# Optimization experiments

Hardware: AMD Instinct MI355X
Metric: run time of the kernel (lower is better)

Reference implementation:

```python
import jax, jax.numpy as jnp
import numpy as np

B, T, D = 4, 2048, 1024
HEADS = 8
D_K = D // HEADS


def setup_inputs() -> dict:
    key = jax.random.key(0)
    kq, kk, kv = jax.random.split(key, 3)
    return {
        "query": jax.random.normal(kq, (B, T, D), dtype=jnp.float32),
        "key": jax.random.normal(kk, (B, T, D), dtype=jnp.float32),
        "value": jax.random.normal(kv, (B, T, D), dtype=jnp.float32),
    }


def reference(query, key, value):
    b, t, d = query.shape
    # [B,T,D] -> [B,H,T,d_k]
    q = query.reshape(b, t, HEADS, D_K).transpose(0, 2, 1, 3)
    k = key.reshape(b, t, HEADS, D_K).transpose(0, 2, 1, 3)
    v = value.reshape(b, t, HEADS, D_K).transpose(0, 2, 1, 3)
    scale = 1.0 / jnp.sqrt(jnp.asarray(D_K, dtype=q.dtype))
    scores = jnp.einsum("bhqd,bhkd->bhqk", q, k) * scale  # [B,H,T,T]
    p_attn = jax.nn.softmax(scores, axis=-1)
    # sharpening: second softmax over 1000*p, clamp to [0,1]
    attn = jnp.clip(jax.nn.softmax(1000.0 * p_attn, axis=-1), 0.0, 1.0)
    x = jnp.einsum("bhqk,bhkd->bhqd", attn, v)  # [B,H,T,d_k]
    out = x.transpose(0, 2, 1, 3).reshape(b, t, HEADS * D_K)
    return out
```

## Files before the change

### kernel.cpp

```cpp
#include <hip/hip_runtime.h>


typedef __attribute__((ext_vector_type(4))) float f32x4;
typedef __attribute__((ext_vector_type(8))) _Float16 h16x8;
typedef __attribute__((ext_vector_type(4))) _Float16 h16x4;
typedef __attribute__((ext_vector_type(8))) short s16x8;
typedef __attribute__((ext_vector_type(4))) short s16x4;
typedef __attribute__((ext_vector_type(2))) unsigned int u32x2;
typedef __attribute__((ext_vector_type(4))) unsigned int u32x4;

#define NB 4
#define T_ 2048
#define D_ 1024
#define NH 8
#define DK 128
#define BQ 64
#define NWG (NB * NH * (T_ / BQ))
#define KB2 32
#define NKC2 (T_ / KB2)
#define SCALE 0.08838834764831845f
#define SC2   0.12751741689839996f
#define MOFF2 11.541560327111707f
#define L2E   1.4426950408889634f

__device__ __forceinline__ unsigned int pk2(float a, float b) {
  return __builtin_bit_cast(unsigned int, __builtin_amdgcn_cvt_pkrtz(a, b));
}
#define H8(p) __builtin_bit_cast(h16x8, *(const s16x8*)(p))

__device__ __forceinline__ void gload16(const unsigned short* g, unsigned short* l) {
  __builtin_amdgcn_global_load_lds(
      (const __attribute__((address_space(1))) void*)g,
      (__attribute__((address_space(3))) void*)l, 16, 0, 0);
}

__global__ __launch_bounds__(256) void cvtK16(const float* __restrict__ Kg,
                                              unsigned short* __restrict__ K16) {
  const int t = threadIdx.x;
#pragma unroll
  for (int i = 0; i < 4; ++i) {
    const unsigned gid = blockIdx.x * 1024u + i * 256u + t;
    const unsigned bhk = gid >> 4, dg = gid & 15u;
    const unsigned b = bhk >> 14, rem = bhk & 16383u;
    const unsigned h = rem >> 11, k = rem & 2047u;
    const float* s = Kg + ((size_t)b * T_ + k) * D_ + h * DK + dg * 8;
    f32x4 x0 = *(const f32x4*)s, x1 = *(const f32x4*)(s + 4);
    h16x8 hv;
#pragma unroll
    for (int j = 0; j < 4; ++j) { hv[j] = (_Float16)x0[j]; hv[j + 4] = (_Float16)x1[j]; }
    *(u32x4*)(K16 + (size_t)gid * 8) = __builtin_bit_cast(u32x4, hv);
  }
}

__global__ __launch_bounds__(256) void trV16(const float* __restrict__ Vg,
                                             unsigned short* __restrict__ V16t) {
  __shared__ float vt[64][129];
  const int t = threadIdx.x;
  const int bh = blockIdx.x >> 5;
  const int kc = blockIdx.x & 31;
  const int b = bh >> 3, h = bh & 7;
  const float* src = Vg + ((size_t)b * T_ + kc * 64) * D_ + h * DK;
#pragma unroll
  for (int p = 0; p < 8; ++p) {
    const int j = t + p * 256;
    const int row = j >> 5, c4 = j & 31;
    f32x4 v = *(const f32x4*)(src + (size_t)row * D_ + c4 * 4);
#pragma unroll
    for (int i = 0; i < 4; ++i) vt[row][c4 * 4 + i] = v[i];
  }
  __syncthreads();
  unsigned short* dst = V16t + (size_t)bh * DK * T_ + (size_t)kc * 64;
#pragma unroll
  for (int i = 0; i < 4; ++i) {
    const int gg = t + i * 256;
    const int d = gg >> 3, kg = gg & 7;
    u32x4 pv;
#pragma unroll
    for (int jj = 0; jj < 4; ++jj)
      pv[jj] = pk2(vt[kg * 8 + 2 * jj][d], vt[kg * 8 + 2 * jj + 1][d]);
    *(u32x4*)(dst + (size_t)d * T_ + kg * 8) = pv;
  }
}

__global__ __launch_bounds__(256, 4) void simattn_v7(
    const float* __restrict__ Qg, const unsigned short* __restrict__ K16,
    const unsigned short* __restrict__ V16t, float* __restrict__ Og) {
  __shared__ __align__(16) unsigned short kf[2][KB2 * DK];
  __shared__ __align__(16) unsigned short vts[2][DK * KB2];

  const int tid  = threadIdx.x;
  const int wid  = tid >> 6;
  const int lane = tid & 63;
  const int lr   = lane & 15;
  const int lg   = lane >> 4;

  const int blk  = (blockIdx.x & 7) * (NWG >> 3) + (blockIdx.x >> 3);
  const int qblk = blk & (T_ / BQ - 1);
  const int h    = (blk >> 5) & (NH - 1);
  const int b    = blk >> 8;
  const int q0   = qblk * BQ;
  const size_t bh  = (size_t)b * (T_ * D_) + (size_t)h * DK;
  const int    bhp = b * NH + h;
  const unsigned short* kp16 = K16 + (size_t)bhp * (T_ * DK);
  const unsigned short* vp16 = V16t + (size_t)bhp * (DK * T_);

  h16x8 qf[4];
  {
    const float* qp = Qg + bh + (size_t)(q0 + wid * 16 + lr) * D_;
#pragma unroll
    for (int s = 0; s < 4; ++s) {
      const int d0 = s * 32 + lg * 8;
      f32x4 x0 = *(const f32x4*)(qp + d0);
      f32x4 x1 = *(const f32x4*)(qp + d0 + 4);
#pragma unroll
      for (int i = 0; i < 4; ++i) {
        qf[s][i]     = (_Float16)x0[i];
        qf[s][i + 4] = (_Float16)x1[i];
      }
    }
  }

  int koffs[2], voffs[2];
  const int kdst0 = wid * 1024;
#pragma unroll
  for (int i = 0; i < 2; ++i) {
    const int id = wid * 2 + i;
    {
      const int r = id * 4 + (lane >> 4), gL = lane & 15;
      koffs[i] = r * DK + ((gL ^ (r & 7)) * 8);
    }
    {
      const int d = id * 16 + (lane >> 2), s = lane & 3;
      voffs[i] = d * T_ + ((s ^ ((d >> 1) & 3)) * 8);
    }
  }
  auto stK = [&](int kc, int buf) {
    const unsigned short* s0 = kp16 + (size_t)kc * (KB2 * DK);
    gload16(s0 + koffs[0], &kf[buf][kdst0]);
    gload16(s0 + koffs[1], &kf[buf][kdst0 + 512]);
  };
  auto stV = [&](int kc, int buf) {
    const unsigned short* s0 = vp16 + kc * KB2;
    gload16(s0 + voffs[0], &vts[buf][kdst0]);
    gload16(s0 + voffs[1], &vts[buf][kdst0 + 512]);
  };

  auto qkT = [&](int buf, f32x4* st) {
    st[0] = (f32x4){0.f, 0.f, 0.f, 0.f};
    st[1] = (f32x4){0.f, 0.f, 0.f, 0.f};
#pragma unroll
    for (int s = 0; s < 4; ++s) {
#pragma unroll
      for (int nt = 0; nt < 2; ++nt) {
        const int kr = nt * 16 + lr;
        const int eg = ((4 * s + lg) ^ (kr & 7)) * 8;
        st[nt] = __builtin_amdgcn_mfma_f32_16x16x32_f16(
            H8(&kf[buf][kr * DK + eg]), qf[s], st[nt], 0, 0, 0);
      }
    }
  };

  float msc = -3.0e38f, l8 = 0.f;
  stK(0, 0);
  __syncthreads();
  for (int kc = 0; kc < NKC2; ++kc) {
    if (kc + 1 < NKC2) stK(kc + 1, (kc + 1) & 1);
    f32x4 st[2];
    qkT(kc & 1, st);
    float e[8];
#pragma unroll
    for (int nt = 0; nt < 2; ++nt) {
#pragma unroll
      for (int r = 0; r < 4; ++r) {
        const float s = st[nt][r];
        msc = fmaxf(msc, s);
        e[nt * 4 + r] = __builtin_amdgcn_exp2f(fmaf(s, SC2, -MOFF2));
      }
    }
    l8 += ((e[0] + e[1]) + (e[2] + e[3])) + ((e[4] + e[5]) + (e[6] + e[7]));
    __syncthreads();
  }
  msc = fmaxf(msc, __shfl_xor(msc, 16));
  msc = fmaxf(msc, __shfl_xor(msc, 32));
  l8 += __shfl_xor(l8, 16);
  l8 += __shfl_xor(l8, 32);
  const float pm   = __builtin_amdgcn_exp2f(fmaf(msc, SC2, -MOFF2));
  const float ul2  = (1000.0f / l8) * L2E;
  const float mcu2 = -ul2 * pm;

  f32x4 y[8];
#pragma unroll
  for (int dt = 0; dt < 8; ++dt) y[dt] = (f32x4){0.f, 0.f, 0.f, 0.f};
  float Wl = 0.f;
  const int src0 = lr + 32 * (lg & 1);
  const int src1 = src0 + 16;
  const bool ntv = (lg >> 1) != 0;

  stK(0, 0);
  stV(0, 0);
  __syncthreads();
  for (int kc = 0; kc < NKC2; ++kc) {
    if (kc + 1 < NKC2) { stK(kc + 1, (kc + 1) & 1); stV(kc + 1, (kc + 1) & 1); }
    const int buf = kc & 1;
    f32x4 st[2];
    qkT(buf, st);

    unsigned pkv[2][2];
#pragma unroll
    for (int nt = 0; nt < 2; ++nt) {
      float w[4];
#pragma unroll
      for (int r = 0; r < 4; ++r) {
        const float pp = __builtin_amdgcn_exp2f(fmaf(st[nt][r], SC2, -MOFF2));
        w[r] = __builtin_amdgcn_exp2f(fmaf(pp, ul2, mcu2));
      }
      Wl += (w[0] + w[1]) + (w[2] + w[3]);
      pkv[nt][0] = pk2(w[0], w[1]);
      pkv[nt][1] = pk2(w[2], w[3]);
    }

    const unsigned a0 = (unsigned)__shfl((int)pkv[0][0], src0);
    const unsigned b0 = (unsigned)__shfl((int)pkv[1][0], src0);
    const unsigned a1 = (unsigned)__shfl((int)pkv[0][1], src0);
    const unsigned b1 = (unsigned)__shfl((int)pkv[1][1], src0);
    const unsigned a2 = (unsigned)__shfl((int)pkv[0][0], src1);
    const unsigned b2 = (unsigned)__shfl((int)pkv[1][0], src1);
    const unsigned a3 = (unsigned)__shfl((int)pkv[0][1], src1);
    const unsigned b3 = (unsigned)__shfl((int)pkv[1][1], src1);
    u32x4 aw;
    aw[0] = ntv ? b0 : a0;
    aw[1] = ntv ? b1 : a1;
    aw[2] = ntv ? b2 : a2;
    aw[3] = ntv ? b3 : a3;
    const h16x8 af = __builtin_bit_cast(h16x8, aw);

#pragma unroll
    for (int dt = 0; dt < 8; ++dt) {
      const int d = dt * 16 + lr;
      const int sv = lg ^ ((d >> 1) & 3);
      y[dt] = __builtin_amdgcn_mfma_f32_16x16x32_f16(
          af, H8(&vts[buf][d * KB2 + sv * 8]), y[dt], 0, 0, 0);
    }
    __syncthreads();
  }

  Wl += __shfl_xor(Wl, 16);
  Wl += __shfl_xor(Wl, 32);
  const float winv = 1.0f / Wl;

  float* op = Og + bh + (size_t)(q0 + wid * 16) * D_;
#pragma unroll
  for (int r = 0; r < 4; ++r) {
    const float wv = __shfl(winv, lg * 4 + r);
#pragma unroll
    for (int dt = 0; dt < 8; ++dt) {
      op[(size_t)(lg * 4 + r) * D_ + dt * 16 + lr] = y[dt][r] * wv;
    }
  }
}

__global__ __launch_bounds__(256, 4) void simattn_fb(
    const float* __restrict__ Qg, const float* __restrict__ Kg,
    const float* __restrict__ Vg, float* __restrict__ Og) {
  __shared__ __align__(16) unsigned short kfb[64][DK];
  __shared__ __align__(16) unsigned short vtb[DK][64];
  __shared__ __align__(16) unsigned int   wlb[4][16][32];

  const int tid  = threadIdx.x;
  const int wid  = tid >> 6;
  const int lane = tid & 63;
  const int lr   = lane & 15;
  const int lg   = lane >> 4;

  const int blk  = blockIdx.x;
  const int qblk = blk & (T_ / BQ - 1);
  const int h    = (blk >> 5) & (NH - 1);
  const int b    = blk >> 8;
  const int q0   = qblk * BQ;
  const size_t bh = (size_t)b * (T_ * D_) + (size_t)h * DK;

  h16x8 qf[4];
  {
    const float* qp = Qg + bh + (size_t)(q0 + wid * 16 + lr) * D_;
#pragma unroll
    for (int s = 0; s < 4; ++s) {
      const int d0 = s * 32 + lg * 8;
      f32x4 x0 = *(const f32x4*)(qp + d0);
      f32x4 x1 = *(const f32x4*)(qp + d0 + 4);
#pragma unroll
      for (int i = 0; i < 4; ++i) { qf[s][i] = (_Float16)x0[i]; qf[s][i+4] = (_Float16)x1[i]; }
    }
  }
  auto stageK = [&](int kc) {
    const float* kp = Kg + bh + (size_t)kc * 64 * D_;
#pragma unroll
    for (int p = 0; p < 8; ++p) {
      const int j = tid + p * 256;
      const int row = j >> 5, c4 = j & 31;
      f32x4 v = *(const f32x4*)(kp + (size_t)row * D_ + c4 * 4);
      h16x4 hv;
#pragma unroll
      for (int i = 0; i < 4; ++i) hv[i] = (_Float16)v[i];
      const int e = (c4 * 4) ^ ((row & 7) << 3);
      *(s16x4*)&kfb[row][e] = __builtin_bit_cast(s16x4, hv);
    }
  };
  auto qkT = [&](f32x4* st) {
#pragma unroll
    for (int nt = 0; nt < 4; ++nt) st[nt] = (f32x4){0.f, 0.f, 0.f, 0.f};
#pragma unroll
    for (int s = 0; s < 4; ++s) {
#pragma unroll
      for (int nt = 0; nt < 4; ++nt) {
        const int kr = nt * 16 + lr;
        const int e = (s * 32 + lg * 8) ^ ((kr & 7) << 3);
        st[nt] = __builtin_amdgcn_mfma_f32_16x16x32_f16(H8(&kfb[kr][e]), qf[s], st[nt], 0, 0, 0);
      }
    }
  };
  float msc = -3.0e38f, l8 = 0.f;
  for (int kc = 0; kc < 32; ++kc) {
    __syncthreads();
    stageK(kc);
    __syncthreads();
    f32x4 st[4];
    qkT(st);
#pragma unroll
    for (int nt = 0; nt < 4; ++nt)
#pragma unroll
      for (int r = 0; r < 4; ++r) {
        const float s = st[nt][r];
        msc = fmaxf(msc, s);
        l8 += __builtin_amdgcn_exp2f(fmaf(s, SC2, -MOFF2));
      }
  }
  msc = fmaxf(msc, __shfl_xor(msc, 16));
  msc = fmaxf(msc, __shfl_xor(msc, 32));
  l8 += __shfl_xor(l8, 16);
  l8 += __shfl_xor(l8, 32);
  const float pm   = __builtin_amdgcn_exp2f(fmaf(msc, SC2, -MOFF2));
  const float ul2  = (1000.0f / l8) * L2E;
  const float mcu2 = -ul2 * pm;

  f32x4 y[8];
#pragma unroll
  for (int dt = 0; dt < 8; ++dt) y[dt] = (f32x4){0.f, 0.f, 0.f, 0.f};
  float Wl = 0.f;
  const int dv  = tid & 127;
  const int kg0 = tid >> 7;
  for (int kc = 0; kc < 32; ++kc) {
    __syncthreads();
    stageK(kc);
    {
      const float* vp = Vg + bh + (size_t)kc * 64 * D_ + dv;
#pragma unroll
      for (int i = 0; i < 4; ++i) {
        const int kg = kg0 + 2 * i;
        const float* vq = vp + (size_t)kg * 8 * D_;
        u32x4 pv;
        pv[0] = pk2(vq[0], vq[D_]);
        pv[1] = pk2(vq[2 * D_], vq[3 * D_]);
        pv[2] = pk2(vq[4 * D_], vq[5 * D_]);
        pv[3] = pk2(vq[6 * D_], vq[7 * D_]);
        *(u32x4*)&vtb[dv][(kg ^ (dv & 7)) * 8] = pv;
      }
    }
    __syncthreads();
    f32x4 st[4];
    qkT(st);
#pragma unroll
    for (int nt = 0; nt < 4; ++nt) {
      float w[4];
#pragma unroll
      for (int r = 0; r < 4; ++r) {
        const float pp = __builtin_amdgcn_exp2f(fmaf(st[nt][r], SC2, -MOFF2));
        w[r] = __builtin_amdgcn_exp2f(fmaf(pp, ul2, mcu2));
      }
      Wl += (w[0] + w[1]) + (w[2] + w[3]);
      u32x2 pk;
      pk[0] = pk2(w[0], w[1]);
      pk[1] = pk2(w[2], w[3]);
      *(u32x2*)&wlb[wid][lr][(nt * 8 + lg * 2) ^ ((lr & 7) << 2)] = pk;
    }
#pragma unroll
    for (int ks = 0; ks < 2; ++ks) {
      h16x8 af = H8((const unsigned short*)&wlb[wid][lr][(ks * 16 + lg * 4) ^ ((lr & 7) << 2)]);
#pragma unroll
      for (int dt = 0; dt < 8; ++dt) {
        const int d = dt * 16 + lr;
        h16x8 vf = H8(&vtb[d][((ks * 4 + lg) ^ (d & 7)) * 8]);
        y[dt] = __builtin_amdgcn_mfma_f32_16x16x32_f16(af, vf, y[dt], 0, 0, 0);
      }
    }
  }
  Wl += __shfl_xor(Wl, 16);
  Wl += __shfl_xor(Wl, 32);
  const float winv = 1.0f / Wl;
  float* op = Og + bh + (size_t)(q0 + wid * 16) * D_;
#pragma unroll
  for (int r = 0; r < 4; ++r) {
    const float wv = __shfl(winv, lg * 4 + r);
#pragma unroll
    for (int dt = 0; dt < 8; ++dt)
      op[(size_t)(lg * 4 + r) * D_ + dt * 16 + lr] = y[dt][r] * wv;
  }
}

extern "C" void kernel_launch(void* const* d_in, const int* in_sizes, int n_in,
                              void* d_out, int out_size, void* d_ws, size_t ws_size,
                              hipStream_t stream) {
  (void)in_sizes; (void)n_in; (void)out_size;
  const float* Q = (const float*)d_in[0];
  const float* K = (const float*)d_in[1];
  const float* V = (const float*)d_in[2];
  float* O = (float*)d_out;
  const size_t half = (size_t)NB * NH * T_ * DK * 2;
  if (ws_size >= 2 * half) {
    unsigned short* K16  = (unsigned short*)d_ws;
    unsigned short* V16t = (unsigned short*)((char*)d_ws + half);
    cvtK16<<<dim3(1024), 256, 0, stream>>>(K, K16);
    trV16<<<dim3(1024), 256, 0, stream>>>(V, V16t);
    simattn_v7<<<dim3(NWG), 256, 0, stream>>>(Q, K16, V16t, O);
  } else {
    simattn_fb<<<dim3(NWG), 256, 0, stream>>>(Q, K, V, O);
  }
}
```

Before: 177.4 us.

## Switch attention kernel to 32x32x16 MFMA with two 32-row waves per block

Rewrites the main attention kernel so each block has two waves, each owning 32 query rows, and uses 32x32x16 f16 MFMA instead of 16x16x32 for both QK^T and PV. This halves threads per block, doubles per-wave K/V staging loads, and replaces the four-way shuffle repacking of probabilities with a single xor-32 exchange. K shared-memory swizzle offsets are adjusted to the new read pattern. The aim is fewer MFMA instructions, more reuse of each LDS fragment, and less shuffle overhead. In exchange each wave holds more accumulator registers, and the launch bounds ask for fewer waves per CU.

```diff
diff --git a/kernel.cpp b/kernel.cpp
--- a/kernel.cpp
+++ b/kernel.cpp
@@ -2,6 +2,7 @@
 
 
 typedef __attribute__((ext_vector_type(4))) float f32x4;
+typedef __attribute__((ext_vector_type(16))) float f32x16;
 typedef __attribute__((ext_vector_type(8))) _Float16 h16x8;
 typedef __attribute__((ext_vector_type(4))) _Float16 h16x4;
 typedef __attribute__((ext_vector_type(8))) short s16x8;
@@ -82,17 +83,18 @@
   }
 }
 
-__global__ __launch_bounds__(256, 4) void simattn_v7(
+__global__ __launch_bounds__(128, 2) void simattn_v8(
     const float* __restrict__ Qg, const unsigned short* __restrict__ K16,
     const unsigned short* __restrict__ V16t, float* __restrict__ Og) {
   __shared__ __align__(16) unsigned short kf[2][KB2 * DK];
   __shared__ __align__(16) unsigned short vts[2][DK * KB2];
 
   const int tid  = threadIdx.x;
-  const int wid  = tid >> 6;
+  const int wid2 = tid >> 6;
   const int lane = tid & 63;
-  const int lr   = lane & 15;
-  const int lg   = lane >> 4;
+  const int c    = lane & 31;
+  const int g    = lane >> 5;
+  const bool hi  = (g != 0);
 
   const int blk  = (blockIdx.x & 7) * (NWG >> 3) + (blockIdx.x >> 3);
   const int qblk = blk & (T_ / BQ - 1);
@@ -104,60 +106,67 @@
   const unsigned short* kp16 = K16 + (size_t)bhp * (T_ * DK);
   const unsigned short* vp16 = V16t + (size_t)bhp * (DK * T_);
 
-  h16x8 qf[4];
+  h16x8 qf[8];
   {
-    const float* qp = Qg + bh + (size_t)(q0 + wid * 16 + lr) * D_;
-#pragma unroll
-    for (int s = 0; s < 4; ++s) {
-      const int d0 = s * 32 + lg * 8;
+    const float* qp = Qg + bh + (size_t)(q0 + wid2 * 32 + c) * D_;
+#pragma unroll
+    for (int step = 0; step < 8; ++step) {
+      const int d0 = step * 16 + g * 8;
       f32x4 x0 = *(const f32x4*)(qp + d0);
       f32x4 x1 = *(const f32x4*)(qp + d0 + 4);
 #pragma unroll
       for (int i = 0; i < 4; ++i) {
-        qf[s][i]     = (_Float16)x0[i];
-        qf[s][i + 4] = (_Float16)x1[i];
-      }
-    }
-  }
-
-  int koffs[2], voffs[2];
-  const int kdst0 = wid * 1024;
-#pragma unroll
-  for (int i = 0; i < 2; ++i) {
-    const int id = wid * 2 + i;
+        qf[step][i]     = (_Float16)x0[i];
+        qf[step][i + 4] = (_Float16)x1[i];
+      }
+    }
+  }
+
+  int koffs[4], voffs[4], ldst[4];
+#pragma unroll
+  for (int i = 0; i < 4; ++i) {
+    const int id = wid2 * 4 + i;
+    ldst[i] = id * 512 + lane * 8;
     {
-      const int r = id * 4 + (lane >> 4), gL = lane & 15;
-      koffs[i] = r * DK + ((gL ^ (r & 7)) * 8);
+      const int r = id * 4 + (lane >> 4), t = lane & 15;
+      const int sk = 4 * ((id >> 1) & 1);
+      koffs[i] = r * DK + ((((t - sk) & 15) ^ (r & 7)) * 8);
     }
     {
-      const int d = id * 16 + (lane >> 2), s = lane & 3;
-      voffs[i] = d * T_ + ((s ^ ((d >> 1) & 3)) * 8);
+      const int d = id * 16 + (lane >> 2), t = lane & 3;
+      voffs[i] = d * T_ + ((t ^ ((d >> 1) & 3)) * 8);
     }
   }
   auto stK = [&](int kc, int buf) {
     const unsigned short* s0 = kp16 + (size_t)kc * (KB2 * DK);
-    gload16(s0 + koffs[0], &kf[buf][kdst0]);
-    gload16(s0 + koffs[1], &kf[buf][kdst0 + 512]);
+#pragma unroll
+    for (int i = 0; i < 4; ++i) gload16(s0 + koffs[i], &kf[buf][ldst[i]]);
   };
   auto stV = [&](int kc, int buf) {
     const unsigned short* s0 = vp16 + kc * KB2;
-    gload16(s0 + voffs[0], &vts[buf][kdst0]);
-    gload16(s0 + voffs[1], &vts[buf][kdst0 + 512]);
+#pragma unroll
+    for (int i = 0; i < 4; ++i) gload16(s0 + voffs[i], &vts[buf][ldst[i]]);
   };
 
-  auto qkT = [&](int buf, f32x4* st) {
-    st[0] = (f32x4){0.f, 0.f, 0.f, 0.f};
-    st[1] = (f32x4){0.f, 0.f, 0.f, 0.f};
-#pragma unroll
-    for (int s = 0; s < 4; ++s) {
-#pragma unroll
-      for (int nt = 0; nt < 2; ++nt) {
-        const int kr = nt * 16 + lr;
-        const int eg = ((4 * s + lg) ^ (kr & 7)) * 8;
-        st[nt] = __builtin_amdgcn_mfma_f32_16x16x32_f16(
-            H8(&kf[buf][kr * DK + eg]), qf[s], st[nt], 0, 0, 0);
-      }
-    }
+  int kread[8];
+  {
+    const int xr = c & 7, skr = 4 * ((c >> 3) & 1);
+#pragma unroll
+    for (int step = 0; step < 8; ++step)
+      kread[step] = c * DK + (((((2 * step + g) ^ xr) + skr) & 15) * 8);
+  }
+  const int vsw = (c >> 1) & 3;
+
+  auto qkT = [&](int buf) {
+    f32x16 st;
+#pragma unroll
+    for (int i = 0; i < 16; ++i) st[i] = 0.f;
+#pragma unroll
+    for (int step = 0; step < 8; ++step) {
+      st = __builtin_amdgcn_mfma_f32_32x32x16_f16(H8(&kf[buf][kread[step]]),
+                                                  qf[step], st, 0, 0, 0);
+    }
+    return st;
   };
 
   float msc = -3.0e38f, l8 = 0.f;
@@ -165,36 +174,33 @@
   __syncthreads();
   for (int kc = 0; kc < NKC2; ++kc) {
     if (kc + 1 < NKC2) stK(kc + 1, (kc + 1) & 1);
-    f32x4 st[2];
-    qkT(kc & 1, st);
-    float e[8];
-#pragma unroll
-    for (int nt = 0; nt < 2; ++nt) {
-#pragma unroll
-      for (int r = 0; r < 4; ++r) {
-        const float s = st[nt][r];
-        msc = fmaxf(msc, s);
-        e[nt * 4 + r] = __builtin_amdgcn_exp2f(fmaf(s, SC2, -MOFF2));
-      }
-    }
-    l8 += ((e[0] + e[1]) + (e[2] + e[3])) + ((e[4] + e[5]) + (e[6] + e[7]));
-    __syncthreads();
-  }
-  msc = fmaxf(msc, __shfl_xor(msc, 16));
+    f32x16 st = qkT(kc & 1);
+    float e[16];
+#pragma unroll
+    for (int r = 0; r < 16; ++r) {
+      msc = fmaxf(msc, st[r]);
+      e[r] = __builtin_amdgcn_exp2f(fmaf(st[r], SC2, -MOFF2));
+    }
+    float s0 = 0.f, s1 = 0.f, s2 = 0.f, s3 = 0.f;
+#pragma unroll
+    for (int r = 0; r < 4; ++r) {
+      s0 += e[r]; s1 += e[4 + r]; s2 += e[8 + r]; s3 += e[12 + r];
+    }
+    l8 += (s0 + s1) + (s2 + s3);
+    __syncthreads();
+  }
   msc = fmaxf(msc, __shfl_xor(msc, 32));
-  l8 += __shfl_xor(l8, 16);
   l8 += __shfl_xor(l8, 32);
   const float pm   = __builtin_amdgcn_exp2f(fmaf(msc, SC2, -MOFF2));
   const float ul2  = (1000.0f / l8) * L2E;
   const float mcu2 = -ul2 * pm;
 
-  f32x4 y[8];
-#pragma unroll
-  for (int dt = 0; dt < 8; ++dt) y[dt] = (f32x4){0.f, 0.f, 0.f, 0.f};
+  f32x16 y[4];
+#pragma unroll
+  for (int dt = 0; dt < 4; ++dt)
+#pragma unroll
+    for (int i = 0; i < 16; ++i) y[dt][i] = 0.f;
   float Wl = 0.f;
-  const int src0 = lr + 32 * (lg & 1);
-  const int src1 = src0 + 16;
-  const bool ntv = (lg >> 1) != 0;
 
   stK(0, 0);
   stV(0, 0);
@@ -202,59 +208,52 @@
   for (int kc = 0; kc < NKC2; ++kc) {
     if (kc + 1 < NKC2) { stK(kc + 1, (kc + 1) & 1); stV(kc + 1, (kc + 1) & 1); }
     const int buf = kc & 1;
-    f32x4 st[2];
-    qkT(buf, st);
-
-    unsigned pkv[2][2];
-#pragma unroll
-    for (int nt = 0; nt < 2; ++nt) {
-      float w[4];
-#pragma unroll
-      for (int r = 0; r < 4; ++r) {
-        const float pp = __builtin_amdgcn_exp2f(fmaf(st[nt][r], SC2, -MOFF2));
-        w[r] = __builtin_amdgcn_exp2f(fmaf(pp, ul2, mcu2));
-      }
-      Wl += (w[0] + w[1]) + (w[2] + w[3]);
-      pkv[nt][0] = pk2(w[0], w[1]);
-      pkv[nt][1] = pk2(w[2], w[3]);
-    }
-
-    const unsigned a0 = (unsigned)__shfl((int)pkv[0][0], src0);
-    const unsigned b0 = (unsigned)__shfl((int)pkv[1][0], src0);
-    const unsigned a1 = (unsigned)__shfl((int)pkv[0][1], src0);
-    const unsigned b1 = (unsigned)__shfl((int)pkv[1][1], src0);
-    const unsigned a2 = (unsigned)__shfl((int)pkv[0][0], src1);
-    const unsigned b2 = (unsigned)__shfl((int)pkv[1][0], src1);
-    const unsigned a3 = (unsigned)__shfl((int)pkv[0][1], src1);
-    const unsigned b3 = (unsigned)__shfl((int)pkv[1][1], src1);
-    u32x4 aw;
-    aw[0] = ntv ? b0 : a0;
-    aw[1] = ntv ? b1 : a1;
-    aw[2] = ntv ? b2 : a2;
-    aw[3] = ntv ? b3 : a3;
-    const h16x8 af = __builtin_bit_cast(h16x8, aw);
-
-#pragma unroll
-    for (int dt = 0; dt < 8; ++dt) {
-      const int d = dt * 16 + lr;
-      const int sv = lg ^ ((d >> 1) & 3);
-      y[dt] = __builtin_amdgcn_mfma_f32_16x16x32_f16(
-          af, H8(&vts[buf][d * KB2 + sv * 8]), y[dt], 0, 0, 0);
-    }
-    __syncthreads();
-  }
-
-  Wl += __shfl_xor(Wl, 16);
+    f32x16 st = qkT(buf);
+
+    unsigned pw[8];
+#pragma unroll
+    for (int m = 0; m < 8; ++m) {
+      const float p0 = __builtin_amdgcn_exp2f(fmaf(st[2 * m], SC2, -MOFF2));
+      const float p1 = __builtin_amdgcn_exp2f(fmaf(st[2 * m + 1], SC2, -MOFF2));
+      const float w0 = __builtin_amdgcn_exp2f(fmaf(p0, ul2, mcu2));
+      const float w1 = __builtin_amdgcn_exp2f(fmaf(p1, ul2, mcu2));
+      Wl += w0 + w1;
+      pw[m] = pk2(w0, w1);
+    }
+
+#pragma unroll
+    for (int hh = 0; hh < 2; ++hh) {
+      const unsigned t0 = hi ? pw[4 * hh] : pw[4 * hh + 2];
+      const unsigned t1 = hi ? pw[4 * hh + 1] : pw[4 * hh + 3];
+      const unsigned r0 = (unsigned)__shfl_xor((int)t0, 32);
+      const unsigned r1 = (unsigned)__shfl_xor((int)t1, 32);
+      u32x4 aw;
+      aw[0] = hi ? r0 : pw[4 * hh];
+      aw[1] = hi ? r1 : pw[4 * hh + 1];
+      aw[2] = hi ? pw[4 * hh + 2] : r0;
+      aw[3] = hi ? pw[4 * hh + 3] : r1;
+      const h16x8 af = __builtin_bit_cast(h16x8, aw);
+#pragma unroll
+      for (int dt = 0; dt < 4; ++dt) {
+        const int d = dt * 32 + c;
+        const h16x8 vf = H8(&vts[buf][d * KB2 + (((2 * hh + g) ^ vsw) * 8)]);
+        y[dt] = __builtin_amdgcn_mfma_f32_32x32x16_f16(af, vf, y[dt], 0, 0, 0);
+      }
+    }
+    __syncthreads();
+  }
+
   Wl += __shfl_xor(Wl, 32);
   const float winv = 1.0f / Wl;
 
-  float* op = Og + bh + (size_t)(q0 + wid * 16) * D_;
-#pragma unroll
-  for (int r = 0; r < 4; ++r) {
-    const float wv = __shfl(winv, lg * 4 + r);
-#pragma unroll
-    for (int dt = 0; dt < 8; ++dt) {
-      op[(size_t)(lg * 4 + r) * D_ + dt * 16 + lr] = y[dt][r] * wv;
+  float* ob = Og + bh + (size_t)(q0 + wid2 * 32) * D_;
+#pragma unroll
+  for (int r = 0; r < 16; ++r) {
+    const int qrow = (r & 3) + 8 * (r >> 2) + 4 * g;
+    const float wv = __shfl(winv, qrow);
+#pragma unroll
+    for (int dt = 0; dt < 4; ++dt) {
+      ob[(size_t)qrow * D_ + dt * 32 + c] = y[dt][r] * wv;
     }
   }
 }
@@ -420,7 +419,7 @@
     unsigned short* V16t = (unsigned short*)((char*)d_ws + half);
     cvtK16<<<dim3(1024), 256, 0, stream>>>(K, K16);
     trV16<<<dim3(1024), 256, 0, stream>>>(V, V16t);
-    simattn_v7<<<dim3(NWG), 256, 0, stream>>>(Q, K16, V16t, O);
+    simattn_v8<<<dim3(NWG), 128, 0, stream>>>(Q, K16, V16t, O);
   } else {
     simattn_fb<<<dim3(NWG), 256, 0, stream>>>(Q, K, V, O);
   }
```

New measurement: 173.1 us. 1.02x faster.
